# Performance work log

Measured on AMD Instinct MI355X. Metric: run time of the kernel, lower is better.

Reference implementation:

```python
import jax, jax.numpy as jnp
import numpy as np

EPS = 1e-8

def setup_inputs() -> dict:
    key = jax.random.key(0)
    k1, k2, k3, k4 = jax.random.split(key, 4)
    B, S, D = 64, 512, 512
    emb1 = jax.random.normal(k1, (B, S, D), dtype=jnp.float32)
    emb2 = jax.random.normal(k2, (B, S, D), dtype=jnp.float32)
    # contiguous prefix attention masks (first n tokens valid), as assumed by the original
    len1 = jax.random.randint(k3, (B,), S // 4, S + 1)
    len2 = jax.random.randint(k4, (B,), S // 4, S + 1)
    pos = jnp.arange(S)
    mask1 = (pos[None, :] < len1[:, None]).astype(jnp.int32)
    mask2 = (pos[None, :] < len2[:, None]).astype(jnp.int32)
    return {"article_1_emb": emb1, "article_2_emb": emb2,
            "article_1_att_mask": mask1, "article_2_att_mask": mask2}


def reference(article_1_emb, article_2_emb, article_1_att_mask, article_2_att_mask):
    # L2-normalize token embeddings (cosine similarity = dot of normalized vectors)
    def l2n(x):
        n = jnp.sqrt(jnp.sum(x * x, axis=-1, keepdims=True))
        return x / jnp.maximum(n, EPS)

    e1 = l2n(article_1_emb)   # [B, S1, D]
    e2 = l2n(article_2_emb)   # [B, S2, D]
    sim = jnp.einsum('bid,bjd->bij', e1, e2)  # [B, S1, S2] pairwise cosine sims

    m1 = article_1_att_mask.astype(jnp.bool_)  # [B, S1]
    m2 = article_2_att_mask.astype(jnp.bool_)  # [B, S2]
    NEG = jnp.float32(-1e9)

    # max over valid j for each valid i, and max over valid i for each valid j
    row_max = jnp.max(jnp.where(m2[:, None, :], sim, NEG), axis=2)  # [B, S1]
    col_max = jnp.max(jnp.where(m1[:, :, None], sim, NEG), axis=1)  # [B, S2]
    row_sum = jnp.sum(jnp.where(m1, row_max, 0.0), axis=1)          # [B]
    col_sum = jnp.sum(jnp.where(m2, col_max, 0.0), axis=1)          # [B]

    n1 = jnp.sum(article_1_att_mask, axis=1).astype(jnp.float32)
    n2 = jnp.sum(article_2_att_mask, axis=1).astype(jnp.float32)
    return (row_sum + col_sum) / (n1 + n2)
```

## Files before the change

### kernel.cpp

```cpp
#include <hip/hip_runtime.h>
#include <hip/hip_bf16.h>


typedef __attribute__((ext_vector_type(8))) short bf16x8;
typedef __attribute__((ext_vector_type(4))) float f32x4;

#define NEGBIG (-1e9f)

__device__ __forceinline__ unsigned packbf2_hw(float lo, float hi) {
    __hip_bfloat162 h = __float22bfloat162_rn(float2{lo, hi});
    union { __hip_bfloat162 h; unsigned u; } c; c.h = h;
    return c.u;
}

#define BAR() do {                                            \
        asm volatile("s_waitcnt lgkmcnt(0)" ::: "memory");    \
        __builtin_amdgcn_s_barrier();                         \
        asm volatile("" ::: "memory");                        \
    } while (0)

__global__ __launch_bounds__(512)
void sim_fused(const float* __restrict__ e1, const float* __restrict__ e2,
               const int* __restrict__ m1g, const int* __restrict__ m2g,
               float* __restrict__ rowmax_p,
               float* __restrict__ colmax_p)
{
    const int bid = blockIdx.x;
    const int l   = ((bid & 7) << 7) | (bid >> 3);
    const int b   = l >> 4;
    const int rt  = l & 3;
    const int ct  = (l >> 2) & 3;

    const int tid  = threadIdx.x;
    const int lane = tid & 63;
    const int w    = tid >> 6;
    const int wm   = w >> 2;
    const int wn   = w & 3;
    const int q    = lane >> 4;
    const int ln   = lane & 15;
    const int nb   = ct * 128;

    __shared__ __align__(16) ushort sA[2][128 * 32];
    __shared__ __align__(16) ushort sB[2][128 * 32];
    float* spr   = reinterpret_cast<float*>(&sA[0][0]);
    float* spc   = reinterpret_cast<float*>(&sA[0][1024]);
    int*   sm1   = reinterpret_cast<int*>(&sA[0][1536]);
    int*   sm2   = reinterpret_cast<int*>(&sA[0][1792]);
    float* sinv1 = reinterpret_cast<float*>(&sB[0][0]);
    float* sinv2 = reinterpret_cast<float*>(&sB[0][256]);

    const int  tt  = tid & 255;
    const int  r   = tt >> 1;
    const int  h   = tt & 1;
    const int  s   = (r ^ (r >> 2)) & 3;
    const bool isA = (tid < 256);
    const float* gsrc = (isA
        ? e1 + ((size_t)(b * 512 + rt * 128 + r)) * 512
        : e2 + ((size_t)(b * 512 + nb + r)) * 512) + h * 16;
    ushort* const wb0 = isA ? &sA[0][0] : &sB[0][0];
    ushort* const wb1 = isA ? &sA[1][0] : &sB[1][0];
    const int wo0 = r * 32 + (((2 * h)     ^ s) << 3);
    const int wo1 = r * 32 + (((2 * h + 1) ^ s) << 3);

    const int sln = (ln & 3) ^ ((ln >> 2) & 3);
    int aoff[4], boff[2];
    #pragma unroll
    for (int mt = 0; mt < 4; ++mt)
        aoff[mt] = (wm * 64 + mt * 16 + ln) * 32 + ((q ^ sln) << 3);
    #pragma unroll
    for (int nt = 0; nt < 2; ++nt)
        boff[nt] = (wn * 32 + nt * 16 + ln) * 32 + ((q ^ sln) << 3);

    float ss = 0.f;
    float4 rg_[2][4];

    auto LOADK = [&](int u, int kf) {
        const float4* p = reinterpret_cast<const float4*>(gsrc + kf);
        rg_[u][0] = p[0]; rg_[u][1] = p[1]; rg_[u][2] = p[2]; rg_[u][3] = p[3];
    };
    auto CVTWRITE = [&](int u, ushort* wb) {
        #pragma unroll
        for (int i = 0; i < 4; ++i) {
            ss += rg_[u][i].x * rg_[u][i].x + rg_[u][i].y * rg_[u][i].y
                + rg_[u][i].z * rg_[u][i].z + rg_[u][i].w * rg_[u][i].w;
        }
        uint4 v;
        v.x = packbf2_hw(rg_[u][0].x, rg_[u][0].y); v.y = packbf2_hw(rg_[u][0].z, rg_[u][0].w);
        v.z = packbf2_hw(rg_[u][1].x, rg_[u][1].y); v.w = packbf2_hw(rg_[u][1].z, rg_[u][1].w);
        *reinterpret_cast<uint4*>(wb + wo0) = v;
        v.x = packbf2_hw(rg_[u][2].x, rg_[u][2].y); v.y = packbf2_hw(rg_[u][2].z, rg_[u][2].w);
        v.z = packbf2_hw(rg_[u][3].x, rg_[u][3].y); v.w = packbf2_hw(rg_[u][3].z, rg_[u][3].w);
        *reinterpret_cast<uint4*>(wb + wo1) = v;
    };

    f32x4 acc[4][2];
    #pragma unroll
    for (int i = 0; i < 4; ++i)
        #pragma unroll
        for (int j = 0; j < 2; ++j)
            acc[i][j] = (f32x4){0.f, 0.f, 0.f, 0.f};

    LOADK(0, 0);
    CVTWRITE(0, wb0);
    LOADK(1, 32);
    BAR();

#define HALF_ITER(P, K)                                                    \
    do {                                                                   \
        if ((K) < 14) LOADK(P, ((K) + 2) * 32);                            \
        bf16x8 af[4], bfr[2];                                              \
        _Pragma("unroll")                                                  \
        for (int mt = 0; mt < 4; ++mt)                                     \
            af[mt] = *reinterpret_cast<const bf16x8*>(&sA[P][aoff[mt]]);   \
        _Pragma("unroll")                                                  \
        for (int nt = 0; nt < 2; ++nt)                                     \
            bfr[nt] = *reinterpret_cast<const bf16x8*>(&sB[P][boff[nt]]);  \
        if ((K) < 15) CVTWRITE((P) ^ 1, ((P) ^ 1) ? wb1 : wb0);            \
        _Pragma("unroll")                                                  \
        for (int mt = 0; mt < 4; ++mt)                                     \
            _Pragma("unroll")                                              \
            for (int nt = 0; nt < 2; ++nt)                                 \
                acc[mt][nt] = __builtin_amdgcn_mfma_f32_16x16x32_bf16(     \
                    af[mt], bfr[nt], acc[mt][nt], 0, 0, 0);                \
        BAR();                                                             \
    } while (0)

    for (int kk = 0; kk < 8; ++kk) {
        HALF_ITER(0, 2 * kk);
        HALF_ITER(1, 2 * kk + 1);
    }
#undef HALF_ITER

    if (tid < 128)      sm1[tid]       = m1g[b * 512 + rt * 128 + tid];
    else if (tid < 256) sm2[tid - 128] = m2g[b * 512 + nb + (tid - 128)];
    ss += __shfl_xor(ss, 1);
    if (h == 0) {
        float inv = 1.0f / fmaxf(sqrtf(ss), 1e-8f);
        if (isA) sinv1[r] = inv;
        else     sinv2[r] = inv;
    }
    BAR();

    float invj[2];
    f32x4 invi[4];
    #pragma unroll
    for (int nt = 0; nt < 2; ++nt)
        invj[nt] = sinv2[wn * 32 + nt * 16 + ln];
    #pragma unroll
    for (int mt = 0; mt < 4; ++mt)
        #pragma unroll
        for (int rg = 0; rg < 4; ++rg)
            invi[mt][rg] = sinv1[wm * 64 + mt * 16 + q * 4 + rg];
    #pragma unroll
    for (int mt = 0; mt < 4; ++mt)
        #pragma unroll
        for (int nt = 0; nt < 2; ++nt)
            acc[mt][nt] = acc[mt][nt] * (invi[mt] * invj[nt]);

    #pragma unroll
    for (int mt = 0; mt < 4; ++mt) {
        #pragma unroll
        for (int rg = 0; rg < 4; ++rg) {
            float rm = NEGBIG;
            #pragma unroll
            for (int nt = 0; nt < 2; ++nt) {
                float v = sm2[wn * 32 + nt * 16 + ln] ? acc[mt][nt][rg] : NEGBIG;
                rm = fmaxf(rm, v);
            }
            rm = fmaxf(rm, __shfl_xor(rm, 1));
            rm = fmaxf(rm, __shfl_xor(rm, 2));
            rm = fmaxf(rm, __shfl_xor(rm, 4));
            rm = fmaxf(rm, __shfl_xor(rm, 8));
            if (ln == 0) spr[wn * 128 + wm * 64 + mt * 16 + q * 4 + rg] = rm;
        }
    }
    #pragma unroll
    for (int nt = 0; nt < 2; ++nt) {
        float cm = NEGBIG;
        #pragma unroll
        for (int mt = 0; mt < 4; ++mt)
            #pragma unroll
            for (int rg = 0; rg < 4; ++rg) {
                float v = sm1[wm * 64 + mt * 16 + q * 4 + rg] ? acc[mt][nt][rg] : NEGBIG;
                cm = fmaxf(cm, v);
            }
        cm = fmaxf(cm, __shfl_xor(cm, 16));
        cm = fmaxf(cm, __shfl_xor(cm, 32));
        if (lane < 16) spc[wm * 128 + wn * 32 + nt * 16 + ln] = cm;
    }
    BAR();
    if (tid < 128) {
        rowmax_p[((size_t)b * 4 + ct) * 512 + rt * 128 + tid] =
            fmaxf(fmaxf(spr[tid], spr[128 + tid]),
                  fmaxf(spr[256 + tid], spr[384 + tid]));
        colmax_p[((size_t)b * 4 + rt) * 512 + nb + tid] =
            fmaxf(spc[tid], spc[128 + tid]);
    }
}

__global__ __launch_bounds__(256)
void final_kernel(const int* __restrict__ m1g, const int* __restrict__ m2g,
                  const float* __restrict__ rowmax_p, const float* __restrict__ colmax_p,
                  float* __restrict__ out)
{
    const int b = blockIdx.x;
    const int tid = threadIdx.x;
    const int lane = tid & 63;
    const int w = tid >> 6;

    float sum = 0.f;
    float nn  = 0.f;
    for (int j = tid; j < 512; j += 256) {
        int mm1 = m1g[b * 512 + j];
        int mm2 = m2g[b * 512 + j];
        nn += (float)(mm1 + mm2);
        const float* rp = rowmax_p + (size_t)b * 2048 + j;
        float rm = fmaxf(fmaxf(rp[0], rp[512]), fmaxf(rp[1024], rp[1536]));
        if (mm1) sum += rm;
        const float* cp = colmax_p + (size_t)b * 2048 + j;
        float cm = fmaxf(fmaxf(cp[0], cp[512]), fmaxf(cp[1024], cp[1536]));
        if (mm2) sum += cm;
    }
    #pragma unroll
    for (int m = 32; m; m >>= 1) {
        sum += __shfl_xor(sum, m);
        nn  += __shfl_xor(nn, m);
    }
    __shared__ float ssum[4], snn[4];
    if (lane == 0) { ssum[w] = sum; snn[w] = nn; }
    __syncthreads();
    if (tid == 0) {
        float S = ssum[0] + ssum[1] + ssum[2] + ssum[3];
        float N = snn[0] + snn[1] + snn[2] + snn[3];
        out[b] = S / N;
    }
}

extern "C" void kernel_launch(void* const* d_in, const int* in_sizes, int n_in,
                              void* d_out, int out_size, void* d_ws, size_t ws_size,
                              hipStream_t stream) {
    const float* e1 = (const float*)d_in[0];
    const float* e2 = (const float*)d_in[1];
    const int*   m1 = (const int*)d_in[2];
    const int*   m2 = (const int*)d_in[3];
    float* out = (float*)d_out;

    float* ws = (float*)d_ws;
    float* rowmax_p = ws;
    float* colmax_p = ws + 131072;

    sim_fused<<<dim3(1024), 512, 0, stream>>>(e1, e2, m1, m2,
                                              rowmax_p, colmax_p);
    final_kernel<<<64, 256, 0, stream>>>(m1, m2, rowmax_p, colmax_p, out);
}
```

Before: 178.7 us.

## Double the K-tile to 64 to halve barriers in the fused similarity GEMM

Each pipeline stage now covers K=64 instead of 32, so the shared buffers double in size and the main loop runs 8 phases instead of 16. Each phase does two MFMA sub-steps, which halves the number of block barriers. The XOR swizzle is widened to 8 chunks to suit the 64-element rows. The global prefetch now comes after the LDS write rather than before the fragment reads, which changes how the load latency overlaps with compute. The costs are more registers (8 float4 prefetch registers) and double the LDS, which may lower occupancy.

```diff
diff --git a/kernel.cpp b/kernel.cpp
--- a/kernel.cpp
+++ b/kernel.cpp
@@ -40,8 +40,8 @@
     const int ln   = lane & 15;
     const int nb   = ct * 128;
 
-    __shared__ __align__(16) ushort sA[2][128 * 32];
-    __shared__ __align__(16) ushort sB[2][128 * 32];
+    __shared__ __align__(16) ushort sA[2][128 * 64];
+    __shared__ __align__(16) ushort sB[2][128 * 64];
     float* spr   = reinterpret_cast<float*>(&sA[0][0]);
     float* spc   = reinterpret_cast<float*>(&sA[0][1024]);
     int*   sm1   = reinterpret_cast<int*>(&sA[0][1536]);
@@ -52,45 +52,59 @@
     const int  tt  = tid & 255;
     const int  r   = tt >> 1;
     const int  h   = tt & 1;
-    const int  s   = (r ^ (r >> 2)) & 3;
+    const int  s3r = ((r >> 3) ^ r) & 7;
     const bool isA = (tid < 256);
     const float* gsrc = (isA
         ? e1 + ((size_t)(b * 512 + rt * 128 + r)) * 512
-        : e2 + ((size_t)(b * 512 + nb + r)) * 512) + h * 16;
+        : e2 + ((size_t)(b * 512 + nb + r)) * 512) + h * 32;
     ushort* const wb0 = isA ? &sA[0][0] : &sB[0][0];
     ushort* const wb1 = isA ? &sA[1][0] : &sB[1][0];
-    const int wo0 = r * 32 + (((2 * h)     ^ s) << 3);
-    const int wo1 = r * 32 + (((2 * h + 1) ^ s) << 3);
-
-    const int sln = (ln & 3) ^ ((ln >> 2) & 3);
-    int aoff[4], boff[2];
-    #pragma unroll
-    for (int mt = 0; mt < 4; ++mt)
-        aoff[mt] = (wm * 64 + mt * 16 + ln) * 32 + ((q ^ sln) << 3);
-    #pragma unroll
-    for (int nt = 0; nt < 2; ++nt)
-        boff[nt] = (wn * 32 + nt * 16 + ln) * 32 + ((q ^ sln) << 3);
+    int wo[4];
+    #pragma unroll
+    for (int j = 0; j < 4; ++j)
+        wo[j] = r * 64 + (((4 * h + j) ^ s3r) << 3);
+
+    int aoff[4][2], boff[2][2];
+    #pragma unroll
+    for (int mt = 0; mt < 4; ++mt) {
+        const int row = wm * 64 + mt * 16 + ln;
+        const int s3  = ((row >> 3) ^ row) & 7;
+        #pragma unroll
+        for (int ks = 0; ks < 2; ++ks)
+            aoff[mt][ks] = row * 64 + (((ks * 4 + q) ^ s3) << 3);
+    }
+    #pragma unroll
+    for (int nt = 0; nt < 2; ++nt) {
+        const int col = wn * 32 + nt * 16 + ln;
+        const int s3  = ((col >> 3) ^ col) & 7;
+        #pragma unroll
+        for (int ks = 0; ks < 2; ++ks)
+            boff[nt][ks] = col * 64 + (((ks * 4 + q) ^ s3) << 3);
+    }
 
     float ss = 0.f;
-    float4 rg_[2][4];
-
-    auto LOADK = [&](int u, int kf) {
+    float4 rg_[8];
+
+    auto LOADK = [&](int kf) {
         const float4* p = reinterpret_cast<const float4*>(gsrc + kf);
-        rg_[u][0] = p[0]; rg_[u][1] = p[1]; rg_[u][2] = p[2]; rg_[u][3] = p[3];
+        #pragma unroll
+        for (int j = 0; j < 8; ++j) rg_[j] = p[j];
     };
-    auto CVTWRITE = [&](int u, ushort* wb) {
-        #pragma unroll
-        for (int i = 0; i < 4; ++i) {
-            ss += rg_[u][i].x * rg_[u][i].x + rg_[u][i].y * rg_[u][i].y
-                + rg_[u][i].z * rg_[u][i].z + rg_[u][i].w * rg_[u][i].w;
+    auto CVTWRITE = [&](ushort* wb) {
+        #pragma unroll
+        for (int i = 0; i < 8; ++i) {
+            ss += rg_[i].x * rg_[i].x + rg_[i].y * rg_[i].y
+                + rg_[i].z * rg_[i].z + rg_[i].w * rg_[i].w;
         }
-        uint4 v;
-        v.x = packbf2_hw(rg_[u][0].x, rg_[u][0].y); v.y = packbf2_hw(rg_[u][0].z, rg_[u][0].w);
-        v.z = packbf2_hw(rg_[u][1].x, rg_[u][1].y); v.w = packbf2_hw(rg_[u][1].z, rg_[u][1].w);
-        *reinterpret_cast<uint4*>(wb + wo0) = v;
-        v.x = packbf2_hw(rg_[u][2].x, rg_[u][2].y); v.y = packbf2_hw(rg_[u][2].z, rg_[u][2].w);
-        v.z = packbf2_hw(rg_[u][3].x, rg_[u][3].y); v.w = packbf2_hw(rg_[u][3].z, rg_[u][3].w);
-        *reinterpret_cast<uint4*>(wb + wo1) = v;
+        #pragma unroll
+        for (int j = 0; j < 4; ++j) {
+            uint4 v;
+            v.x = packbf2_hw(rg_[2*j].x,   rg_[2*j].y);
+            v.y = packbf2_hw(rg_[2*j].z,   rg_[2*j].w);
+            v.z = packbf2_hw(rg_[2*j+1].x, rg_[2*j+1].y);
+            v.w = packbf2_hw(rg_[2*j+1].z, rg_[2*j+1].w);
+            *reinterpret_cast<uint4*>(wb + wo[j]) = v;
+        }
     };
 
     f32x4 acc[4][2];
@@ -100,22 +114,34 @@
         for (int j = 0; j < 2; ++j)
             acc[i][j] = (f32x4){0.f, 0.f, 0.f, 0.f};
 
-    LOADK(0, 0);
-    CVTWRITE(0, wb0);
-    LOADK(1, 32);
+    LOADK(0);
+    CVTWRITE(wb0);
+    LOADK(64);
     BAR();
 
-#define HALF_ITER(P, K)                                                    \
+#define PHASE(P, T)                                                        \
     do {                                                                   \
-        if ((K) < 14) LOADK(P, ((K) + 2) * 32);                            \
         bf16x8 af[4], bfr[2];                                              \
         _Pragma("unroll")                                                  \
         for (int mt = 0; mt < 4; ++mt)                                     \
-            af[mt] = *reinterpret_cast<const bf16x8*>(&sA[P][aoff[mt]]);   \
+            af[mt] = *reinterpret_cast<const bf16x8*>(&sA[P][aoff[mt][0]]);\
         _Pragma("unroll")                                                  \
         for (int nt = 0; nt < 2; ++nt)                                     \
-            bfr[nt] = *reinterpret_cast<const bf16x8*>(&sB[P][boff[nt]]);  \
-        if ((K) < 15) CVTWRITE((P) ^ 1, ((P) ^ 1) ? wb1 : wb0);            \
+            bfr[nt] = *reinterpret_cast<const bf16x8*>(&sB[P][boff[nt][0]]);\
+        if ((T) < 7) CVTWRITE((P) ? wb0 : wb1);                            \
+        if ((T) < 6) LOADK(((T) + 2) * 64);                                \
+        _Pragma("unroll")                                                  \
+        for (int mt = 0; mt < 4; ++mt)                                     \
+            _Pragma("unroll")                                              \
+            for (int nt = 0; nt < 2; ++nt)                                 \
+                acc[mt][nt] = __builtin_amdgcn_mfma_f32_16x16x32_bf16(     \
+                    af[mt], bfr[nt], acc[mt][nt], 0, 0, 0);                \
+        _Pragma("unroll")                                                  \
+        for (int mt = 0; mt < 4; ++mt)                                     \
+            af[mt] = *reinterpret_cast<const bf16x8*>(&sA[P][aoff[mt][1]]);\
+        _Pragma("unroll")                                                  \
+        for (int nt = 0; nt < 2; ++nt)                                     \
+            bfr[nt] = *reinterpret_cast<const bf16x8*>(&sB[P][boff[nt][1]]);\
         _Pragma("unroll")                                                  \
         for (int mt = 0; mt < 4; ++mt)                                     \
             _Pragma("unroll")                                              \
@@ -125,11 +151,11 @@
         BAR();                                                             \
     } while (0)
 
-    for (int kk = 0; kk < 8; ++kk) {
-        HALF_ITER(0, 2 * kk);
-        HALF_ITER(1, 2 * kk + 1);
-    }
-#undef HALF_ITER
+    for (int kk = 0; kk < 4; ++kk) {
+        PHASE(0, 2 * kk);
+        PHASE(1, 2 * kk + 1);
+    }
+#undef PHASE
 
     if (tid < 128)      sm1[tid]       = m1g[b * 512 + rt * 128 + tid];
     else if (tid < 256) sm2[tid - 128] = m2g[b * 512 + nb + (tid - 128)];
```

After: 200.8 us. +12.4%, slower.
